# Kernel optimization log

Measured on AMD Instinct MI355X. Metric: run time of the kernel, lower is better.

Reference implementation:

```python
import jax, jax.numpy as jnp
import numpy as np

D_MODEL = 1024
MAX_ELEMENTS = 128


def setup_inputs() -> dict:
    key = jax.random.key(0)
    ks = jax.random.split(key, 12)
    B, S = 256, 128
    d, dq = D_MODEL, D_MODEL // 4
    inp = {
        "element_types": jax.random.randint(ks[0], (B, S), 0, 5, dtype=jnp.int64 if jax.config.jax_enable_x64 else jnp.int32),
        "element_indices": jax.random.randint(ks[1], (B, S), 0, MAX_ELEMENTS, dtype=jnp.int64 if jax.config.jax_enable_x64 else jnp.int32),
        "style_vectors": jax.random.normal(ks[2], (B, 5), dtype=jnp.float32),
        "page_captions": jax.random.normal(ks[3], (B, 768), dtype=jnp.float32),
        # learned parameters (torch Linear stored as [in, out] so y = x @ W + b)
        "type_emb": jax.random.normal(ks[4], (5, d), dtype=jnp.float32) * 0.02,
        "pos_emb": jax.random.normal(ks[5], (MAX_ELEMENTS, d), dtype=jnp.float32) * 0.02,
        "style_w1": jax.random.normal(ks[6], (5, dq), dtype=jnp.float32) * 0.02,
        "style_b1": jnp.zeros((dq,), dtype=jnp.float32),
        "style_w2": jax.random.normal(ks[7], (dq, d), dtype=jnp.float32) * 0.02,
        "style_b2": jnp.zeros((d,), dtype=jnp.float32),
        "text_w": jax.random.normal(ks[8], (768, d), dtype=jnp.float32) * 0.02,
        "text_b": jnp.zeros((d,), dtype=jnp.float32),
        "final_pos_emb": jax.random.normal(ks[9], (MAX_ELEMENTS, d), dtype=jnp.float32) * 0.02,
    }
    return inp


def reference(element_types, element_indices, style_vectors, page_captions,
              type_emb, pos_emb, style_w1, style_b1, style_w2, style_b2,
              text_w, text_b, final_pos_emb):
    B, S = element_types.shape
    # table gathers: [B, S, d]
    emb = type_emb[element_types] + pos_emb[element_indices]
    # per-batch style/text embeds computed ONCE (the torch loop recomputes them per step)
    style_embed = jnp.maximum(style_vectors @ style_w1 + style_b1, 0.0) @ style_w2 + style_b2  # [B, d]
    page_embed = page_captions @ text_w + text_b  # [B, d]
    # loop over i with mask (types[:, i] == 1) == broadcast masked add
    mask1 = (element_types == 1)[:, :, None]  # [B, S, 1]
    emb = emb + mask1 * (style_embed + page_embed)[:, None, :]
    # final positional encoding over positions 0..S-1
    emb = emb + final_pos_emb[:S][None, :, :]
    padding_mask = element_types == 0
    return emb, padding_mask
```

## Files before the change

### kernel.cpp

```cpp
#include <hip/hip_runtime.h>

#define D      1024
#define SEQ    128
#define BATCH  256
#define DQ     256
#define TEXTC  768

typedef float f32x4 __attribute__((ext_vector_type(4)));
typedef float f32x2 __attribute__((ext_vector_type(2)));

__global__ __launch_bounds__(256) void gemm_fused(
    const float* __restrict__ style_vectors,
    const float* __restrict__ page_captions,
    const float* __restrict__ style_w1,
    const float* __restrict__ style_b1,
    const float* __restrict__ style_w2,
    const float* __restrict__ style_b2,
    const float* __restrict__ text_w,
    const float* __restrict__ text_b,
    float* __restrict__ part)
{
    __shared__ float As[16][36];
    __shared__ float Bs[16][68];

    const int m0  = blockIdx.x * 32;
    const int n0  = blockIdx.y * 64;
    const int z   = blockIdx.z;
    const int tid = threadIdx.x;
    const int tm  = tid >> 4;
    const int tn  = tid & 15;

    const int am = tid >> 2;
    const int ak = (tid & 3) * 4;

    float sv[5];
    if (z == 0 && tid < 128) {
#pragma unroll
        for (int j = 0; j < 5; ++j) sv[j] = style_vectors[(m0 + am) * 5 + j];
    }

    float acc[2][4] = {};

    for (int kc = 0; kc < 256; kc += 16) {
        if (tid < 128) {
            if (z == 0) {
                int k = kc + ak;
#pragma unroll
                for (int r = 0; r < 4; ++r) {
                    float h = style_b1[k + r];
#pragma unroll
                    for (int j = 0; j < 5; ++j)
                        h = fmaf(sv[j], style_w1[j * DQ + k + r], h);
                    As[ak + r][am] = fmaxf(h, 0.0f);
                }
            } else {
                float4 av = *(const float4*)
                    &page_captions[(m0 + am) * TEXTC + (z * 256 - DQ) + kc + ak];
                As[ak + 0][am] = av.x;
                As[ak + 1][am] = av.y;
                As[ak + 2][am] = av.z;
                As[ak + 3][am] = av.w;
            }
        }
        {
            int kk   = tid >> 4;
            int nq   = (tid & 15) * 4;
            int krow = z * 256 + kc + kk;
            const float* Wrow = (z == 0) ? &style_w2[krow * D]
                                         : &text_w[(krow - DQ) * D];
            *(float4*)&Bs[kk][nq] = *(const float4*)&Wrow[n0 + nq];
        }
        __syncthreads();

#pragma unroll
        for (int kk = 0; kk < 16; ++kk) {
            f32x2 a2 = *(const f32x2*)&As[kk][tm * 2];
            f32x4 b4 = *(const f32x4*)&Bs[kk][tn * 4];
#pragma unroll
            for (int ii = 0; ii < 2; ++ii)
#pragma unroll
                for (int jj = 0; jj < 4; ++jj)
                    acc[ii][jj] = fmaf(a2[ii], b4[jj], acc[ii][jj]);
        }
        __syncthreads();
    }

    float* dst = part + (size_t)z * BATCH * D;
    const int n = n0 + tn * 4;
#pragma unroll
    for (int ii = 0; ii < 2; ++ii) {
        int m = m0 + tm * 2 + ii;
        f32x4 v = {acc[ii][0], acc[ii][1], acc[ii][2], acc[ii][3]};
        if (z == 0) {
            v[0] += style_b2[n + 0] + text_b[n + 0];
            v[1] += style_b2[n + 1] + text_b[n + 1];
            v[2] += style_b2[n + 2] + text_b[n + 2];
            v[3] += style_b2[n + 3] + text_b[n + 3];
        }
        *(f32x4*)&dst[m * D + n] = v;
    }
}

__global__ __launch_bounds__(256) void reduce_part(
    const float* __restrict__ part,
    float* __restrict__ comb)
{
    const int i = blockIdx.x * 256 + threadIdx.x;
    const f32x4* p = (const f32x4*)part;
    const int Q = BATCH * D / 4;
    f32x4 v = __builtin_nontemporal_load(&p[i])
            + __builtin_nontemporal_load(&p[i + Q])
            + __builtin_nontemporal_load(&p[i + 2 * Q])
            + __builtin_nontemporal_load(&p[i + 3 * Q]);
    ((f32x4*)comb)[i] = v;
}

__global__ __launch_bounds__(256) void scatter_kernel(
    const int* __restrict__ types,
    const int* __restrict__ indices,
    const float* __restrict__ type_emb,
    const float* __restrict__ pos_emb,
    const float* __restrict__ final_pos_emb,
    const float* __restrict__ comb,
    float* __restrict__ out_emb,
    float* __restrict__ out_mask)
{
    const int tid  = threadIdx.x;
    const int wave = tid >> 6;
    const int lane = tid & 63;
    const int bs   = blockIdx.x * 4 + wave;
    const int b    = bs >> 7;
    const int s    = bs & 127;
    const int et   = types[bs];
    const int ei   = indices[bs];

    const f32x4* te = (const f32x4*)&type_emb[et * D];
    const f32x4* pe = (const f32x4*)&pos_emb[ei * D];
    const f32x4* fe = (const f32x4*)&final_pos_emb[s * D];
    f32x4* dst = (f32x4*)out_emb + (size_t)bs * 256;

    if (et == 1) {
        const f32x4* cb = (const f32x4*)&comb[b * D];
#pragma unroll
        for (int j = 0; j < 4; ++j) {
            int idx = lane + 64 * j;
            f32x4 v = te[idx] + pe[idx] + fe[idx] + cb[idx];
            __builtin_nontemporal_store(v, &dst[idx]);
        }
    } else {
#pragma unroll
        for (int j = 0; j < 4; ++j) {
            int idx = lane + 64 * j;
            f32x4 v = te[idx] + pe[idx] + fe[idx];
            __builtin_nontemporal_store(v, &dst[idx]);
        }
    }

    if (lane == 0)
        out_mask[bs] = (et == 0) ? 1.0f : 0.0f;
}

extern "C" void kernel_launch(void* const* d_in, const int* in_sizes, int n_in,
                              void* d_out, int out_size, void* d_ws, size_t ws_size,
                              hipStream_t stream) {
    const int*   element_types   = (const int*)  d_in[0];
    const int*   element_indices = (const int*)  d_in[1];
    const float* style_vectors   = (const float*)d_in[2];
    const float* page_captions   = (const float*)d_in[3];
    const float* type_emb        = (const float*)d_in[4];
    const float* pos_emb         = (const float*)d_in[5];
    const float* style_w1        = (const float*)d_in[6];
    const float* style_b1        = (const float*)d_in[7];
    const float* style_w2        = (const float*)d_in[8];
    const float* style_b2        = (const float*)d_in[9];
    const float* text_w          = (const float*)d_in[10];
    const float* text_b          = (const float*)d_in[11];
    const float* final_pos_emb   = (const float*)d_in[12];

    float* part = (float*)d_ws;
    float* comb = (float*)d_ws + 4 * BATCH * D;

    float* out_emb  = (float*)d_out;
    float* out_mask = (float*)d_out + BATCH * SEQ * D;

    gemm_fused<<<dim3(BATCH / 32, D / 64, 4), 256, 0, stream>>>(
        style_vectors, page_captions, style_w1, style_b1,
        style_w2, style_b2, text_w, text_b, part);

    reduce_part<<<BATCH * D / 4 / 256, 256, 0, stream>>>(part, comb);

    scatter_kernel<<<BATCH * SEQ / 4, 256, 0, stream>>>(
        element_types, element_indices, type_emb, pos_emb, final_pos_emb,
        comb, out_emb, out_mask);
}
```

Baseline: 202.4 us.

## Fuse split-K partial reduction into scatter and double GEMM k-tile depth

Removes the separate reduce_part kernel and has the scatter kernel sum the four split-K partial buffers directly for rows whose type is 1. The GEMM k-tile grows from 16 to 32, so all 256 threads load A and there are half as many barrier iterations. This saves one launch and one write-then-read pass over the combined buffer. In exchange, each type-1 row rereads four partials instead of one combined vector, which adds more reads in the scatter kernel.

```diff
diff --git a/kernel.cpp b/kernel.cpp
--- a/kernel.cpp
+++ b/kernel.cpp
@@ -20,8 +20,8 @@
     const float* __restrict__ text_b,
     float* __restrict__ part)
 {
-    __shared__ float As[16][36];
-    __shared__ float Bs[16][68];
+    __shared__ float As[32][36];
+    __shared__ float Bs[32][68];
 
     const int m0  = blockIdx.x * 32;
     const int n0  = blockIdx.y * 64;
@@ -30,50 +30,52 @@
     const int tm  = tid >> 4;
     const int tn  = tid & 15;
 
-    const int am = tid >> 2;
-    const int ak = (tid & 3) * 4;
+    const int am = tid >> 3;
+    const int ak = (tid & 7) * 4;
 
     float sv[5];
-    if (z == 0 && tid < 128) {
+    if (z == 0) {
 #pragma unroll
         for (int j = 0; j < 5; ++j) sv[j] = style_vectors[(m0 + am) * 5 + j];
     }
 
     float acc[2][4] = {};
 
-    for (int kc = 0; kc < 256; kc += 16) {
-        if (tid < 128) {
-            if (z == 0) {
-                int k = kc + ak;
+    for (int kc = 0; kc < 256; kc += 32) {
+        if (z == 0) {
+            int k = kc + ak;
 #pragma unroll
-                for (int r = 0; r < 4; ++r) {
-                    float h = style_b1[k + r];
+            for (int r = 0; r < 4; ++r) {
+                float h = style_b1[k + r];
 #pragma unroll
-                    for (int j = 0; j < 5; ++j)
-                        h = fmaf(sv[j], style_w1[j * DQ + k + r], h);
-                    As[ak + r][am] = fmaxf(h, 0.0f);
-                }
-            } else {
-                float4 av = *(const float4*)
-                    &page_captions[(m0 + am) * TEXTC + (z * 256 - DQ) + kc + ak];
-                As[ak + 0][am] = av.x;
-                As[ak + 1][am] = av.y;
-                As[ak + 2][am] = av.z;
-                As[ak + 3][am] = av.w;
+                for (int j = 0; j < 5; ++j)
+                    h = fmaf(sv[j], style_w1[j * DQ + k + r], h);
+                As[ak + r][am] = fmaxf(h, 0.0f);
             }
+        } else {
+            float4 av = *(const float4*)
+                &page_captions[(m0 + am) * TEXTC + (z * 256 - DQ) + kc + ak];
+            As[ak + 0][am] = av.x;
+            As[ak + 1][am] = av.y;
+            As[ak + 2][am] = av.z;
+            As[ak + 3][am] = av.w;
         }
         {
-            int kk   = tid >> 4;
-            int nq   = (tid & 15) * 4;
-            int krow = z * 256 + kc + kk;
-            const float* Wrow = (z == 0) ? &style_w2[krow * D]
-                                         : &text_w[(krow - DQ) * D];
-            *(float4*)&Bs[kk][nq] = *(const float4*)&Wrow[n0 + nq];
+            int kk = tid >> 4;
+            int nq = (tid & 15) * 4;
+#pragma unroll
+            for (int h = 0; h < 2; ++h) {
+                int kl   = kk + 16 * h;
+                int krow = z * 256 + kc + kl;
+                const float* Wrow = (z == 0) ? &style_w2[krow * D]
+                                             : &text_w[(krow - DQ) * D];
+                *(f32x4*)&Bs[kl][nq] = *(const f32x4*)&Wrow[n0 + nq];
+            }
         }
         __syncthreads();
 
 #pragma unroll
-        for (int kk = 0; kk < 16; ++kk) {
+        for (int kk = 0; kk < 32; ++kk) {
             f32x2 a2 = *(const f32x2*)&As[kk][tm * 2];
             f32x4 b4 = *(const f32x4*)&Bs[kk][tn * 4];
 #pragma unroll
@@ -101,27 +103,13 @@
     }
 }
 
-__global__ __launch_bounds__(256) void reduce_part(
-    const float* __restrict__ part,
-    float* __restrict__ comb)
-{
-    const int i = blockIdx.x * 256 + threadIdx.x;
-    const f32x4* p = (const f32x4*)part;
-    const int Q = BATCH * D / 4;
-    f32x4 v = __builtin_nontemporal_load(&p[i])
-            + __builtin_nontemporal_load(&p[i + Q])
-            + __builtin_nontemporal_load(&p[i + 2 * Q])
-            + __builtin_nontemporal_load(&p[i + 3 * Q]);
-    ((f32x4*)comb)[i] = v;
-}
-
 __global__ __launch_bounds__(256) void scatter_kernel(
     const int* __restrict__ types,
     const int* __restrict__ indices,
     const float* __restrict__ type_emb,
     const float* __restrict__ pos_emb,
     const float* __restrict__ final_pos_emb,
-    const float* __restrict__ comb,
+    const float* __restrict__ part,
     float* __restrict__ out_emb,
     float* __restrict__ out_mask)
 {
@@ -140,11 +128,13 @@
     f32x4* dst = (f32x4*)out_emb + (size_t)bs * 256;
 
     if (et == 1) {
-        const f32x4* cb = (const f32x4*)&comb[b * D];
+        const int Q = BATCH * D / 4;
+        const f32x4* pp = (const f32x4*)part + b * 256;
 #pragma unroll
         for (int j = 0; j < 4; ++j) {
             int idx = lane + 64 * j;
-            f32x4 v = te[idx] + pe[idx] + fe[idx] + cb[idx];
+            f32x4 v = te[idx] + pe[idx] + fe[idx]
+                    + pp[idx] + pp[idx + Q] + pp[idx + 2 * Q] + pp[idx + 3 * Q];
             __builtin_nontemporal_store(v, &dst[idx]);
         }
     } else {
@@ -178,7 +168,6 @@
     const float* final_pos_emb   = (const float*)d_in[12];
 
     float* part = (float*)d_ws;
-    float* comb = (float*)d_ws + 4 * BATCH * D;
 
     float* out_emb  = (float*)d_out;
     float* out_mask = (float*)d_out + BATCH * SEQ * D;
@@ -187,9 +176,7 @@
         style_vectors, page_captions, style_w1, style_b1,
         style_w2, style_b2, text_w, text_b, part);
 
-    reduce_part<<<BATCH * D / 4 / 256, 256, 0, stream>>>(part, comb);
-
     scatter_kernel<<<BATCH * SEQ / 4, 256, 0, stream>>>(
         element_types, element_indices, type_emb, pos_emb, final_pos_emb,
-        comb, out_emb, out_mask);
+        part, out_emb, out_mask);
 }
```

After: 199.3 us. Within noise of the previous version (-1.5%).
